# Kernel tuning notes

Hardware: AMD Instinct MI355X
Metric: run time of the kernel (lower is better)

Reference implementation:

```python
import jax, jax.numpy as jnp
import numpy as np

B, T, M, DK, DV, S = 64, 256, 64, 128, 256, 128
NSK, NQ = 200, 2000


def _glorot(k, shape):
    lim = np.sqrt(6.0 / (shape[0] + shape[1])).astype(np.float32)
    return jax.random.uniform(k, shape, jnp.float32, -lim, lim)


def setup_inputs() -> dict:
    key = jax.random.key(0)
    ks = jax.random.split(key, 16)
    tn = lambda k, shape: 0.1 * jax.random.truncated_normal(k, -2.0, 2.0, shape, jnp.float32)
    return {
        "q_data": jax.random.randint(ks[0], (B, T), 0, NSK + 1),
        "qa_data": jax.random.randint(ks[1], (B, T), 0, 2 * NSK + 1),
        "s_data": jax.random.randint(ks[2], (B, T), 0, NQ + 1),
        "key_memory": tn(ks[3], (M, DK)),
        "value_memory": tn(ks[4], (M, DV)),
        "Eq": 0.05 * jax.random.normal(ks[5], (NSK + 1, DK), jnp.float32),
        "Eqa": 0.05 * jax.random.normal(ks[6], (2 * NSK + 1, DV), jnp.float32),
        "Es": 0.05 * jax.random.normal(ks[7], (NQ + 1, DK), jnp.float32),
        "We": _glorot(ks[8], (DV, DV)), "be": jnp.zeros((DV,), jnp.float32),
        "Wa": _glorot(ks[9], (DV, DV)), "ba": jnp.zeros((DV,), jnp.float32),
        "Wsa": _glorot(ks[10], (DV, M)), "bsa": jnp.zeros((M,), jnp.float32),
        "Wqd1": _glorot(ks[11], (DK, S)), "bqd1": jnp.zeros((S,), jnp.float32),
        "Wqd": _glorot(ks[12], (S, 1)), "bqd": jnp.zeros((1,), jnp.float32),
        "Wsd1": _glorot(ks[13], (DK, S)), "bsd1": jnp.zeros((S,), jnp.float32),
        "Wsd": _glorot(ks[14], (S, 1)), "bsd": jnp.zeros((1,), jnp.float32),
    }


def reference(q_data, qa_data, s_data, key_memory, value_memory, Eq, Eqa, Es,
              We, be, Wa, ba, Wsa, bsa, Wqd1, bqd1, Wqd, bqd, Wsd1, bsd1, Wsd, bsd):
    b = q_data.shape[0]
    qe = Eq[q_data]    # [B,T,DK]
    qae = Eqa[qa_data]  # [B,T,DV]
    se = Es[s_data]    # [B,T,DK]
    # time-independent precomputation (same math, hoisted out of the loop)
    corr = jax.nn.softmax(jnp.einsum("btk,mk->btm", qe, key_memory), axis=-1)  # [B,T,M]
    erase = qae @ We + be  # [B,T,DV] (activation=None in source)
    add = qae @ Wa + ba    # [B,T,DV]
    qd = jnp.tanh(qe @ Wqd1 + bqd1) @ Wqd + bqd  # [B,T,1]
    sd = jnp.tanh(se @ Wsd1 + bsd1) @ Wsd + bsd  # [B,T,1]

    def step(Mv, x):
        cw, er, ad = x  # [B,M], [B,DV], [B,DV]
        read = jnp.einsum("bm,bmd->bd", cw, Mv)        # read BEFORE write
        sa1 = read @ Wsa + bsa                          # [B,M]
        sa = jnp.sum(cw * sa1, axis=1)                  # [B]
        scale = cw[:, :, None]                          # [B,M,1]
        Mv_new = Mv * (1.0 - er[:, None, :] * scale) + ad[:, None, :] * scale
        return Mv_new, sa

    Mv0 = jnp.broadcast_to(value_memory[None], (b,) + value_memory.shape)
    xs = (corr.transpose(1, 0, 2), erase.transpose(1, 0, 2), add.transpose(1, 0, 2))
    _, sa_t = jax.lax.scan(step, Mv0, xs)  # sa_t: [T,B]
    z = 3.0 * sa_t.T - qd[..., 0] - sd[..., 0]  # [B,T]
    return jax.nn.sigmoid(z)
```

## Files before the change

### kernel.cpp

```cpp
#include <hip/hip_runtime.h>
#include <math.h>

#define B_   64
#define T_   256
#define M_   64
#define DK_  128
#define DV_  256
#define S_   128
#define NQR  201
#define NQAR 401
#define NSR  2001

static __device__ __forceinline__ int imin(int a, int b){ return a < b ? a : b; }

static __device__ __forceinline__ float fast_tanh(float x){
  float e = __expf(2.f * x);
  return 1.f - 2.f / (e + 1.f);
}

template<int CTRL, int RM>
static __device__ __forceinline__ float dppadd(float x) {
  return x + __int_as_float(
      __builtin_amdgcn_update_dpp(0, __float_as_int(x), CTRL, RM, 0xf, true));
}
static __device__ __forceinline__ float wave_sum_lane63(float x) {
  x = dppadd<0x111, 0xf>(x);
  x = dppadd<0x112, 0xf>(x);
  x = dppadd<0x114, 0xf>(x);
  x = dppadd<0x118, 0xf>(x);
  x = dppadd<0x142, 0xa>(x);
  x = dppadd<0x143, 0xc>(x);
  return x;
}
static __device__ __forceinline__ float row_sum_lane15(float x) {
  x = dppadd<0x111, 0xf>(x);
  x = dppadd<0x112, 0xf>(x);
  x = dppadd<0x114, 0xf>(x);
  x = dppadd<0x118, 0xf>(x);
  return x;
}

__device__ void corr_role(int blk, const float* __restrict__ Eq,
                          const float* __restrict__ Km,
                          const float* __restrict__ Wsa,
                          const float* __restrict__ bsa,
                          float* __restrict__ corr,
                          float* __restrict__ w2_t,
                          float* __restrict__ csb_t)
{
  __shared__ float eq[4][DK_];
  __shared__ float cwb[4][M_];
  const int w = threadIdx.x >> 6, m = threadIdx.x & 63;
  const int i  = blk * 4 + w;
  const int ic = imin(i, NQR - 1);
  eq[w][m]      = Eq[ic * DK_ + m];
  eq[w][m + 64] = Eq[ic * DK_ + 64 + m];
  float acc = 0.f;
  const float4* kr = (const float4*)(Km + m * DK_);
  #pragma unroll 8
  for (int k4 = 0; k4 < DK_ / 4; ++k4) {
    float4 kv = kr[k4];
    acc = fmaf(eq[w][k4 * 4 + 0], kv.x, acc);
    acc = fmaf(eq[w][k4 * 4 + 1], kv.y, acc);
    acc = fmaf(eq[w][k4 * 4 + 2], kv.z, acc);
    acc = fmaf(eq[w][k4 * 4 + 3], kv.w, acc);
  }
  float mx = acc;
  #pragma unroll
  for (int off = 32; off; off >>= 1) mx = fmaxf(mx, __shfl_xor(mx, off, 64));
  float e = __expf(acc - mx);
  float ssum = e;
  #pragma unroll
  for (int off = 32; off; off >>= 1) ssum += __shfl_xor(ssum, off, 64);
  const float cw = e / ssum;
  if (i < NQR) corr[i * M_ + m] = cw;
  cwb[w][m] = cw;

  float pv = wave_sum_lane63(cw * bsa[m]);
  if (m == 63 && i < NQR) csb_t[i] = pv;

  float aw[4] = {0,0,0,0};
  for (int mm4 = 0; mm4 < M_ / 4; ++mm4) {
    #pragma unroll
    for (int r = 0; r < 4; ++r) {
      float4 wv = *(const float4*)(Wsa + (r * 64 + m) * M_ + mm4 * 4);
      aw[r] = fmaf(cwb[w][mm4 * 4 + 0], wv.x, aw[r]);
      aw[r] = fmaf(cwb[w][mm4 * 4 + 1], wv.y, aw[r]);
      aw[r] = fmaf(cwb[w][mm4 * 4 + 2], wv.z, aw[r]);
      aw[r] = fmaf(cwb[w][mm4 * 4 + 3], wv.w, aw[r]);
    }
  }
  if (i < NQR) {
    #pragma unroll
    for (int r = 0; r < 4; ++r) w2_t[i * DV_ + r * 64 + m] = aw[r];
  }
}

__device__ void ea_role(int blk, const float* __restrict__ Eqa,
                        const float* __restrict__ We, const float* __restrict__ be,
                        const float* __restrict__ Wa, const float* __restrict__ ba,
                        float* __restrict__ eat)
{
  __shared__ float a[8][DV_];
  const int d  = threadIdx.x;
  const int i0 = blk * 8;
  #pragma unroll
  for (int r = 0; r < 8; ++r) a[r][d] = Eqa[imin(i0 + r, NQAR - 1) * DV_ + d];
  __syncthreads();
  float er[8] = {0,0,0,0,0,0,0,0}, ad[8] = {0,0,0,0,0,0,0,0};
  for (int k = 0; k < DV_; ++k) {
    float we = We[k * DV_ + d];
    float wa = Wa[k * DV_ + d];
    #pragma unroll
    for (int r = 0; r < 8; ++r) {
      er[r] = fmaf(a[r][k], we, er[r]);
      ad[r] = fmaf(a[r][k], wa, ad[r]);
    }
  }
  const float beo = be[d], bao = ba[d];
  #pragma unroll
  for (int r = 0; r < 8; ++r) {
    int i = i0 + r;
    if (i < NQAR) {
      float2 v; v.x = er[r] + beo; v.y = ad[r] + bao;
      *(float2*)(eat + (size_t)(i * DV_ + d) * 2) = v;
    }
  }
}

__device__ void mlp_role(int blk, const float* __restrict__ E,
                         const float* __restrict__ W1, const float* __restrict__ b1,
                         const float* __restrict__ W2v, const float* __restrict__ b2,
                         float* __restrict__ outt, int nrows)
{
  __shared__ float e[8 * S_];
  __shared__ float red[8][2];
  const int tid = threadIdx.x;
  const int s = tid & 127, rh = tid >> 7;
  const int i0 = blk * 8;
  #pragma unroll
  for (int j = 0; j < 4; ++j) {
    int x = tid + j * 256;
    int row = imin(i0 + (x >> 7), nrows - 1);
    e[x] = E[row * DK_ + (x & 127)];
  }
  __syncthreads();
  float acc[4] = {0,0,0,0};
  const float* eb = e + rh * 4 * 128;
  for (int k = 0; k < DK_; ++k) {
    float wv = W1[k * S_ + s];
    #pragma unroll
    for (int r = 0; r < 4; ++r) acc[r] = fmaf(eb[r * 128 + k], wv, acc[r]);
  }
  const float b1s = b1[s], w2s = W2v[s];
  float p[4];
  #pragma unroll
  for (int r = 0; r < 4; ++r) p[r] = fast_tanh(acc[r] + b1s) * w2s;
  #pragma unroll
  for (int r = 0; r < 4; ++r) p[r] = wave_sum_lane63(p[r]);
  const int lane = tid & 63;
  const int half = s >> 6;
  if (lane == 63) {
    #pragma unroll
    for (int r = 0; r < 4; ++r) red[rh * 4 + r][half] = p[r];
  }
  __syncthreads();
  if (tid < 8) {
    int i = i0 + tid;
    if (i < nrows) outt[i] = red[tid][0] + red[tid][1] + b2[0];
  }
}

__device__ void pk_role(int blk, const int* __restrict__ q,
                        const int* __restrict__ qa, int* __restrict__ pkt)
{
  const int i = (blk * 256 + threadIdx.x) * 4;
  int4 qv = *(const int4*)(q + i);
  int4 av = *(const int4*)(qa + i);
  int4 p;
  p.x = (av.x << 16) | qv.x;
  p.y = (av.y << 16) | qv.y;
  p.z = (av.z << 16) | qv.z;
  p.w = (av.w << 16) | qv.w;
  *(int4*)(pkt + i) = p;
}

#define NB_CORR 51
#define NB_EA   51
#define NB_QD   26
#define NB_SD   251
#define NB_PK   16
#define NB_TOT  (NB_CORR + NB_EA + NB_QD + NB_SD + NB_PK)

__global__ __launch_bounds__(256) void tables_kernel(
    const int* q_data, const int* qa_data, int* pkt,
    const float* Eq, const float* Km, const float* Wsa, const float* bsa,
    float* corr_t, float* w2_t, float* csb_t,
    const float* Eqa, const float* We, const float* be,
    const float* Wa, const float* ba, float* eat,
    const float* Wqd1, const float* bqd1, const float* Wqd, const float* bqd, float* qd_t,
    const float* Es, const float* Wsd1, const float* bsd1, const float* Wsd, const float* bsd, float* sd_t)
{
  int blk = blockIdx.x;
  if (blk < NB_CORR) { corr_role(blk, Eq, Km, Wsa, bsa, corr_t, w2_t, csb_t); return; }
  blk -= NB_CORR;
  if (blk < NB_EA)   { ea_role(blk, Eqa, We, be, Wa, ba, eat); return; }
  blk -= NB_EA;
  if (blk < NB_QD)   { mlp_role(blk, Eq, Wqd1, bqd1, Wqd, bqd, qd_t, NQR); return; }
  blk -= NB_QD;
  if (blk < NB_SD)   { mlp_role(blk, Es, Wsd1, bsd1, Wsd, bsd, sd_t, NSR); return; }
  blk -= NB_SD;
  pk_role(blk, q_data, qa_data, pkt);
}

struct VOps { float2 ea0, ea1; float w20, w21; };

static __device__ __forceinline__ int4 getpk(const int4& pk, int g) {
  int4 r;
  r.x = __builtin_amdgcn_readlane(pk.x, g);
  r.y = __builtin_amdgcn_readlane(pk.y, g);
  r.z = __builtin_amdgcn_readlane(pk.z, g);
  r.w = __builtin_amdgcn_readlane(pk.w, g);
  return r;
}
#define PQ(v)  ((v) & 0xffff)
#define PA(v)  ((int)(((unsigned)(v)) >> 16))

static __device__ __forceinline__ void fetch_c(
    const int4& P, int m0, const float* __restrict__ corr_t,
    float4 (&cA)[2][4], float4 (&cB)[2][4])
{
  const float4* p0 = (const float4*)(corr_t + PQ(P.x) * M_ + m0);
  const float4* p1 = (const float4*)(corr_t + PQ(P.y) * M_ + m0);
  const float4* p2 = (const float4*)(corr_t + PQ(P.z) * M_ + m0);
  const float4* p3 = (const float4*)(corr_t + PQ(P.w) * M_ + m0);
  #pragma unroll
  for (int k = 0; k < 4; ++k) {
    cA[0][k] = p0[k];
    cA[1][k] = p1[k];
    cB[0][k] = p2[k];
    cB[1][k] = p3[k];
  }
}

static __device__ __forceinline__ void fetch_v(
    const int4& P, int d, const float* __restrict__ eat,
    const float* __restrict__ w2_t, VOps& A, VOps& B)
{
  A.ea0 = *(const float2*)(eat + (size_t)(PA(P.x) * DV_ + d) * 2);
  A.ea1 = *(const float2*)(eat + (size_t)(PA(P.y) * DV_ + d) * 2);
  B.ea0 = *(const float2*)(eat + (size_t)(PA(P.z) * DV_ + d) * 2);
  B.ea1 = *(const float2*)(eat + (size_t)(PA(P.w) * DV_ + d) * 2);
  A.w20 = w2_t[PQ(P.x) * DV_ + d];
  A.w21 = w2_t[PQ(P.y) * DV_ + d];
  B.w20 = w2_t[PQ(P.z) * DV_ + d];
  B.w21 = w2_t[PQ(P.w) * DV_ + d];
}

static __device__ __forceinline__ float stepf(
    float (&Mv)[16], const float4 (&c)[4], float2 ea, float w2)
{
  const float er = ea.x, ad = ea.y;
  float r0 = c[0].x * Mv[0];
  float r1 = c[0].y * Mv[1];
  #pragma unroll
  for (int k = 0; k < 4; ++k) {
    const float cx = c[k].x, cy = c[k].y, cz = c[k].z, cw = c[k].w;
    if (k > 0) {
      r0 = fmaf(cx, Mv[4 * k + 0], r0);
      r1 = fmaf(cy, Mv[4 * k + 1], r1);
    }
    Mv[4 * k + 0] = fmaf(cx, fmaf(-er, Mv[4 * k + 0], ad), Mv[4 * k + 0]);
    Mv[4 * k + 1] = fmaf(cy, fmaf(-er, Mv[4 * k + 1], ad), Mv[4 * k + 1]);
    r0 = fmaf(cz, Mv[4 * k + 2], r0);
    r1 = fmaf(cw, Mv[4 * k + 3], r1);
    Mv[4 * k + 2] = fmaf(cz, fmaf(-er, Mv[4 * k + 2], ad), Mv[4 * k + 2]);
    Mv[4 * k + 3] = fmaf(cw, fmaf(-er, Mv[4 * k + 3], ad), Mv[4 * k + 3]);
  }
  return row_sum_lane15((r0 + r1) * w2);
}

__global__ __launch_bounds__(256) void scan_kernel(
    const int* __restrict__ pkt,
    const float* __restrict__ corr_t, const float* __restrict__ eat,
    const float* __restrict__ w2_t,
    const float* __restrict__ Vm, float* __restrict__ sa_part)
{
  const int b   = blockIdx.y;
  const int dq  = blockIdx.x;
  const int tid = threadIdx.x;
  const int dl  = tid & 63;
  const int mg  = tid >> 6;
  const int m0  = __builtin_amdgcn_readfirstlane(mg * 16);
  const int d   = dq * 64 + dl;
  const int sub = dl >> 4;

  const int4 pk = ((const int4*)(pkt + b * T_))[dl];

  float Mv[16];
  #pragma unroll
  for (int j = 0; j < 16; ++j) Mv[j] = Vm[(m0 + j) * DV_ + d];

  float* baseP = sa_part + ((dq * 16 + mg * 4 + sub) * B_ + b) * T_;

  int4 I0 = getpk(pk, 0);
  int4 I1 = getpk(pk, 1);
  float4 cA[2][4], cB[2][4];
  VOps VEa, VEb, VOa, VOb;
  fetch_c(I0, m0, corr_t, cA, cB);
  fetch_v(I0, d, eat, w2_t, VEa, VEb);
  fetch_v(I1, d, eat, w2_t, VOa, VOb);
  int4 Icur = I1;
  int4 Inxt = getpk(pk, 2);

  for (int i = 0; i < 64; i += 2) {
    float4 p;
    p.x = stepf(Mv, cA[0], VEa.ea0, VEa.w20);
    p.y = stepf(Mv, cA[1], VEa.ea1, VEa.w21);
    p.z = stepf(Mv, cB[0], VEb.ea0, VEb.w20);
    p.w = stepf(Mv, cB[1], VEb.ea1, VEb.w21);
    fetch_c(Icur, m0, corr_t, cA, cB);
    fetch_v(Inxt, d, eat, w2_t, VEa, VEb);
    Icur = Inxt;
    Inxt = getpk(pk, (i + 3) & 63);
    if ((dl & 15) == 15) *(float4*)(baseP + 4 * i) = p;

    p.x = stepf(Mv, cA[0], VOa.ea0, VOa.w20);
    p.y = stepf(Mv, cA[1], VOa.ea1, VOa.w21);
    p.z = stepf(Mv, cB[0], VOb.ea0, VOb.w20);
    p.w = stepf(Mv, cB[1], VOb.ea1, VOb.w21);
    fetch_c(Icur, m0, corr_t, cA, cB);
    fetch_v(Inxt, d, eat, w2_t, VOa, VOb);
    Icur = Inxt;
    Inxt = getpk(pk, (i + 4) & 63);
    if ((dl & 15) == 15) *(float4*)(baseP + 4 * i + 4) = p;
  }
}

__global__ __launch_bounds__(256) void final_kernel(
    const int* __restrict__ q_data, const int* __restrict__ s_data,
    const float* __restrict__ sa_part, const float* __restrict__ csb_t,
    const float* __restrict__ qd_t, const float* __restrict__ sd_t,
    float* __restrict__ out)
{
  const int b = blockIdx.x, t = threadIdx.x;
  float s = 0.f;
  #pragma unroll
  for (int p = 0; p < 64; ++p) s += sa_part[(p * B_ + b) * T_ + t];
  const int bt = b * T_ + t;
  const int q  = q_data[bt];
  const int si = s_data[bt];
  const float sa = s + csb_t[q];
  const float z = 3.f * sa - qd_t[q] - sd_t[si];
  out[bt] = 1.f / (1.f + __expf(-z));
}

extern "C" void kernel_launch(void* const* d_in, const int* in_sizes, int n_in,
                              void* d_out, int out_size, void* d_ws, size_t ws_size,
                              hipStream_t stream)
{
  const int*   q_data = (const int*)d_in[0];
  const int*   qa_data= (const int*)d_in[1];
  const int*   s_data = (const int*)d_in[2];
  const float* Km     = (const float*)d_in[3];
  const float* Vm     = (const float*)d_in[4];
  const float* Eq     = (const float*)d_in[5];
  const float* Eqa    = (const float*)d_in[6];
  const float* Es     = (const float*)d_in[7];
  const float* We     = (const float*)d_in[8];
  const float* be     = (const float*)d_in[9];
  const float* Wa     = (const float*)d_in[10];
  const float* ba     = (const float*)d_in[11];
  const float* Wsa    = (const float*)d_in[12];
  const float* bsa    = (const float*)d_in[13];
  const float* Wqd1   = (const float*)d_in[14];
  const float* bqd1   = (const float*)d_in[15];
  const float* Wqd    = (const float*)d_in[16];
  const float* bqd    = (const float*)d_in[17];
  const float* Wsd1   = (const float*)d_in[18];
  const float* bsd1   = (const float*)d_in[19];
  const float* Wsd    = (const float*)d_in[20];
  const float* bsd    = (const float*)d_in[21];
  float* out = (float*)d_out;

  float* wsf    = (float*)d_ws;
  float* corr_t = wsf;
  float* w2_t   = corr_t + NQR * M_;
  float* csb_t  = w2_t + NQR * DV_;
  float* eat    = csb_t + 204;
  float* qd_t   = eat + NQAR * DV_ * 2;
  float* sd_t   = qd_t + 204;
  int*   pkt    = (int*)(sd_t + 2004);
  float* sa_p   = sd_t + 2004 + 16384;

  tables_kernel<<<NB_TOT, 256, 0, stream>>>(
      q_data, qa_data, pkt,
      Eq, Km, Wsa, bsa, corr_t, w2_t, csb_t,
      Eqa, We, be, Wa, ba, eat,
      Wqd1, bqd1, Wqd, bqd, qd_t,
      Es, Wsd1, bsd1, Wsd, bsd, sd_t);
  scan_kernel<<<dim3(4, B_), 256, 0, stream>>>(pkt, corr_t, eat, w2_t, Vm, sa_p);
  final_kernel<<<B_, 256, 0, stream>>>(q_data, s_data, sa_p, csb_t, qd_t, sd_t, out);
}
```

Baseline: 165.5 us.

## Split scan memory rows across eight waves with 8 rows per thread

Doubles the scan block to 512 threads so each wave owns 8 memory slots instead of 16. This halves the per-step serial FMA chain per thread and increases active waves. The per-step reduction widens to 32 lanes, with one write per half-wave, so the partial count stays at 64. Per-step index and load overhead per thread is unchanged, so latency of the fetch pipeline may dominate.

```diff
diff --git a/kernel.cpp b/kernel.cpp
--- a/kernel.cpp
+++ b/kernel.cpp
@@ -32,11 +32,12 @@
   x = dppadd<0x143, 0xc>(x);
   return x;
 }
-static __device__ __forceinline__ float row_sum_lane15(float x) {
+static __device__ __forceinline__ float half_sum_lane31_63(float x) {
   x = dppadd<0x111, 0xf>(x);
   x = dppadd<0x112, 0xf>(x);
   x = dppadd<0x114, 0xf>(x);
   x = dppadd<0x118, 0xf>(x);
+  x = dppadd<0x142, 0xa>(x);
   return x;
 }
 
@@ -228,19 +229,16 @@
 
 static __device__ __forceinline__ void fetch_c(
     const int4& P, int m0, const float* __restrict__ corr_t,
-    float4 (&cA)[2][4], float4 (&cB)[2][4])
+    float4 (&cA)[2][2], float4 (&cB)[2][2])
 {
   const float4* p0 = (const float4*)(corr_t + PQ(P.x) * M_ + m0);
   const float4* p1 = (const float4*)(corr_t + PQ(P.y) * M_ + m0);
   const float4* p2 = (const float4*)(corr_t + PQ(P.z) * M_ + m0);
   const float4* p3 = (const float4*)(corr_t + PQ(P.w) * M_ + m0);
-  #pragma unroll
-  for (int k = 0; k < 4; ++k) {
-    cA[0][k] = p0[k];
-    cA[1][k] = p1[k];
-    cB[0][k] = p2[k];
-    cB[1][k] = p3[k];
-  }
+  cA[0][0] = p0[0];  cA[0][1] = p0[1];
+  cA[1][0] = p1[0];  cA[1][1] = p1[1];
+  cB[0][0] = p2[0];  cB[0][1] = p2[1];
+  cB[1][0] = p3[0];  cB[1][1] = p3[1];
 }
 
 static __device__ __forceinline__ void fetch_v(
@@ -258,29 +256,29 @@
 }
 
 static __device__ __forceinline__ float stepf(
-    float (&Mv)[16], const float4 (&c)[4], float2 ea, float w2)
+    float (&Mv)[8], const float4& c0, const float4& c1, float2 ea, float w2)
 {
   const float er = ea.x, ad = ea.y;
-  float r0 = c[0].x * Mv[0];
-  float r1 = c[0].y * Mv[1];
-  #pragma unroll
-  for (int k = 0; k < 4; ++k) {
-    const float cx = c[k].x, cy = c[k].y, cz = c[k].z, cw = c[k].w;
-    if (k > 0) {
-      r0 = fmaf(cx, Mv[4 * k + 0], r0);
-      r1 = fmaf(cy, Mv[4 * k + 1], r1);
-    }
-    Mv[4 * k + 0] = fmaf(cx, fmaf(-er, Mv[4 * k + 0], ad), Mv[4 * k + 0]);
-    Mv[4 * k + 1] = fmaf(cy, fmaf(-er, Mv[4 * k + 1], ad), Mv[4 * k + 1]);
-    r0 = fmaf(cz, Mv[4 * k + 2], r0);
-    r1 = fmaf(cw, Mv[4 * k + 3], r1);
-    Mv[4 * k + 2] = fmaf(cz, fmaf(-er, Mv[4 * k + 2], ad), Mv[4 * k + 2]);
-    Mv[4 * k + 3] = fmaf(cw, fmaf(-er, Mv[4 * k + 3], ad), Mv[4 * k + 3]);
-  }
-  return row_sum_lane15((r0 + r1) * w2);
-}
-
-__global__ __launch_bounds__(256) void scan_kernel(
+  float r0 = c0.x * Mv[0];
+  float r1 = c0.y * Mv[1];
+  Mv[0] = fmaf(c0.x, fmaf(-er, Mv[0], ad), Mv[0]);
+  Mv[1] = fmaf(c0.y, fmaf(-er, Mv[1], ad), Mv[1]);
+  r0 = fmaf(c0.z, Mv[2], r0);
+  r1 = fmaf(c0.w, Mv[3], r1);
+  Mv[2] = fmaf(c0.z, fmaf(-er, Mv[2], ad), Mv[2]);
+  Mv[3] = fmaf(c0.w, fmaf(-er, Mv[3], ad), Mv[3]);
+  r0 = fmaf(c1.x, Mv[4], r0);
+  r1 = fmaf(c1.y, Mv[5], r1);
+  Mv[4] = fmaf(c1.x, fmaf(-er, Mv[4], ad), Mv[4]);
+  Mv[5] = fmaf(c1.y, fmaf(-er, Mv[5], ad), Mv[5]);
+  r0 = fmaf(c1.z, Mv[6], r0);
+  r1 = fmaf(c1.w, Mv[7], r1);
+  Mv[6] = fmaf(c1.z, fmaf(-er, Mv[6], ad), Mv[6]);
+  Mv[7] = fmaf(c1.w, fmaf(-er, Mv[7], ad), Mv[7]);
+  return half_sum_lane31_63((r0 + r1) * w2);
+}
+
+__global__ __launch_bounds__(512) void scan_kernel(
     const int* __restrict__ pkt,
     const float* __restrict__ corr_t, const float* __restrict__ eat,
     const float* __restrict__ w2_t,
@@ -291,21 +289,21 @@
   const int tid = threadIdx.x;
   const int dl  = tid & 63;
   const int mg  = tid >> 6;
-  const int m0  = __builtin_amdgcn_readfirstlane(mg * 16);
+  const int m0  = __builtin_amdgcn_readfirstlane(mg * 8);
   const int d   = dq * 64 + dl;
-  const int sub = dl >> 4;
+  const int half = dl >> 5;
 
   const int4 pk = ((const int4*)(pkt + b * T_))[dl];
 
-  float Mv[16];
-  #pragma unroll
-  for (int j = 0; j < 16; ++j) Mv[j] = Vm[(m0 + j) * DV_ + d];
-
-  float* baseP = sa_part + ((dq * 16 + mg * 4 + sub) * B_ + b) * T_;
+  float Mv[8];
+  #pragma unroll
+  for (int j = 0; j < 8; ++j) Mv[j] = Vm[(m0 + j) * DV_ + d];
+
+  float* baseP = sa_part + ((dq * 16 + mg * 2 + half) * B_ + b) * T_;
 
   int4 I0 = getpk(pk, 0);
   int4 I1 = getpk(pk, 1);
-  float4 cA[2][4], cB[2][4];
+  float4 cA[2][2], cB[2][2];
   VOps VEa, VEb, VOa, VOb;
   fetch_c(I0, m0, corr_t, cA, cB);
   fetch_v(I0, d, eat, w2_t, VEa, VEb);
@@ -315,25 +313,25 @@
 
   for (int i = 0; i < 64; i += 2) {
     float4 p;
-    p.x = stepf(Mv, cA[0], VEa.ea0, VEa.w20);
-    p.y = stepf(Mv, cA[1], VEa.ea1, VEa.w21);
-    p.z = stepf(Mv, cB[0], VEb.ea0, VEb.w20);
-    p.w = stepf(Mv, cB[1], VEb.ea1, VEb.w21);
+    p.x = stepf(Mv, cA[0][0], cA[0][1], VEa.ea0, VEa.w20);
+    p.y = stepf(Mv, cA[1][0], cA[1][1], VEa.ea1, VEa.w21);
+    p.z = stepf(Mv, cB[0][0], cB[0][1], VEb.ea0, VEb.w20);
+    p.w = stepf(Mv, cB[1][0], cB[1][1], VEb.ea1, VEb.w21);
     fetch_c(Icur, m0, corr_t, cA, cB);
     fetch_v(Inxt, d, eat, w2_t, VEa, VEb);
     Icur = Inxt;
     Inxt = getpk(pk, (i + 3) & 63);
-    if ((dl & 15) == 15) *(float4*)(baseP + 4 * i) = p;
-
-    p.x = stepf(Mv, cA[0], VOa.ea0, VOa.w20);
-    p.y = stepf(Mv, cA[1], VOa.ea1, VOa.w21);
-    p.z = stepf(Mv, cB[0], VOb.ea0, VOb.w20);
-    p.w = stepf(Mv, cB[1], VOb.ea1, VOb.w21);
+    if ((dl & 31) == 31) *(float4*)(baseP + 4 * i) = p;
+
+    p.x = stepf(Mv, cA[0][0], cA[0][1], VOa.ea0, VOa.w20);
+    p.y = stepf(Mv, cA[1][0], cA[1][1], VOa.ea1, VOa.w21);
+    p.z = stepf(Mv, cB[0][0], cB[0][1], VOb.ea0, VOb.w20);
+    p.w = stepf(Mv, cB[1][0], cB[1][1], VOb.ea1, VOb.w21);
     fetch_c(Icur, m0, corr_t, cA, cB);
     fetch_v(Inxt, d, eat, w2_t, VOa, VOb);
     Icur = Inxt;
     Inxt = getpk(pk, (i + 4) & 63);
-    if ((dl & 15) == 15) *(float4*)(baseP + 4 * i + 4) = p;
+    if ((dl & 31) == 31) *(float4*)(baseP + 4 * i + 4) = p;
   }
 }
 
@@ -399,6 +397,6 @@
       Eqa, We, be, Wa, ba, eat,
       Wqd1, bqd1, Wqd, bqd, qd_t,
       Es, Wsd1, bsd1, Wsd, bsd, sd_t);
-  scan_kernel<<<dim3(4, B_), 256, 0, stream>>>(pkt, corr_t, eat, w2_t, Vm, sa_p);
+  scan_kernel<<<dim3(4, B_), 512, 0, stream>>>(pkt, corr_t, eat, w2_t, Vm, sa_p);
   final_kernel<<<B_, 256, 0, stream>>>(q_data, s_data, sa_p, csb_t, qd_t, sd_t, out);
 }
```

After: 167.3 us. Within noise of the previous version (+1.1%).
